# Optimization experiments

Measured on AMD Instinct MI355X. Metric: run time of the kernel, lower is better.

## Reference

```python
import jax, jax.numpy as jnp
import numpy as np

BN_EPS = 1e-5


def setup_inputs() -> dict:
    key = jax.random.key(0)
    ks = jax.random.split(key, 4)
    N, V, C = 64, 512, 512
    K, OUT = 2, 512
    x = jax.random.normal(ks[0], (N, V, C), dtype=jnp.float32)
    A = jax.random.uniform(ks[1], (N, K, V, V), dtype=jnp.float32) / V
    conv_w = jax.random.normal(ks[2], (2 * OUT, C), dtype=jnp.float32) / np.sqrt(C)
    conv_b = jax.random.normal(ks[3], (2 * OUT,), dtype=jnp.float32) * 0.01
    gamma = jnp.ones((2 * OUT,), dtype=jnp.float32)
    beta = jnp.zeros((2 * OUT,), dtype=jnp.float32)
    eps_p = jnp.zeros((1,), dtype=jnp.float32)
    return {"x": x, "A": A, "conv_w": conv_w, "conv_b": conv_b,
            "gamma": gamma, "beta": beta, "eps_p": eps_p}


def reference(x, A, conv_w, conv_b, gamma, beta, eps_p):
    # x: (N, V, C); A: (N, K, V, V)
    N, V, C = x.shape
    K = A.shape[1]
    # 1x1 Conv1d over nodes: (N, 2*out, V)
    h = jnp.einsum('nvc,oc->nov', x, conv_w) + conv_b[None, :, None]
    # BatchNorm1d, training-mode batch stats (biased variance, per channel)
    mean = jnp.mean(h, axis=(0, 2), keepdims=True)
    var = jnp.var(h, axis=(0, 2), keepdims=True)
    h = (h - mean) * jax.lax.rsqrt(var + BN_EPS) * gamma[None, :, None] + beta[None, :, None]
    c2 = h.shape[1]
    h = h.reshape(N, K, c2 // K, V)  # (N, K, out, V)
    # graph propagation: x A then (x A) A^T, contracted over node dims
    t = jnp.einsum('nkcm,nkme->nkce', h, A)
    At = jnp.transpose(A, (0, 1, 3, 2))
    y = jnp.einsum('nkce,nkem->ncm', t, At)  # (N, out, V)
    out = (1.0 + eps_p[0]) * x + jnp.transpose(y, (0, 2, 1))
    return out, At
```

## Files before the change

kernel.cpp:

```cpp
#include <hip/hip_runtime.h>
#include <stdint.h>

typedef __bf16 bf16x8 __attribute__((ext_vector_type(8)));
typedef float f32x4 __attribute__((ext_vector_type(4)));
typedef unsigned short us4_t __attribute__((ext_vector_type(4)));
typedef unsigned short us8_t __attribute__((ext_vector_type(8)));

__device__ __forceinline__ unsigned short f2bf(float f) {
  __bf16 b = (__bf16)f;
  return __builtin_bit_cast(unsigned short, b);
}
__device__ __forceinline__ float bf2f(unsigned short u) {
  union { uint32_t u; float f; } v; v.u = ((uint32_t)u) << 16;
  return v.f;
}

__device__ __forceinline__ void gload16(const void* g, void* l) {
  __builtin_amdgcn_global_load_lds(
      (const __attribute__((address_space(1))) void*)g,
      (__attribute__((address_space(3))) void*)l, 16, 0, 0);
}

__device__ __forceinline__ void stage_tile(const unsigned short* g, size_t ldg,
                                           unsigned short* lds, int wid, int lane) {
#pragma unroll
  for (int i = 0; i < 2; ++i) {
    int seg = wid * 2 + i;
    const unsigned short* gp = g + (size_t)(seg * 16 + (lane >> 2)) * ldg + (lane & 3) * 8;
    gload16(gp, lds + seg * 512);
  }
}

__device__ __forceinline__ void mfma_step(const unsigned short* As, const unsigned short* Bs,
                                          int ldb, f32x4 (*acc)[4],
                                          int wr, int wc, int lr, int lk) {
  bf16x8 a[4], b[4];
#pragma unroll
  for (int mi = 0; mi < 4; ++mi)
    a[mi] = *(const bf16x8*)(As + (wr + mi * 16 + lr) * 32 + lk * 8);
#pragma unroll
  for (int ni = 0; ni < 4; ++ni)
    b[ni] = *(const bf16x8*)(Bs + (wc + ni * 16 + lr) * ldb + lk * 8);
#pragma unroll
  for (int mi = 0; mi < 4; ++mi)
#pragma unroll
    for (int ni = 0; ni < 4; ++ni)
      acc[mi][ni] = __builtin_amdgcn_mfma_f32_16x16x32_bf16(a[mi], b[ni], acc[mi][ni], 0, 0, 0);
}

__device__ __forceinline__ void bn_block(
    const unsigned short* __restrict__ H, const float* __restrict__ gamma,
    const float* __restrict__ beta, float* __restrict__ sc_sh,
    int o, int tid, float* r1, float* r2) {
  const int g = tid >> 6, l = tid & 63;
  float s1 = 0.f, s2 = 0.f;
  for (int step = 0; step < 16; ++step) {
    int n = g + step * 4;
    const us8_t* row = (const us8_t*)(H + ((size_t)n * 1024 + o) * 512);
    us8_t v = row[l];
#pragma unroll
    for (int j = 0; j < 8; ++j) { float f = bf2f(v[j]); s1 += f; s2 += f * f; }
  }
  r1[tid] = s1; r2[tid] = s2;
  __syncthreads();
  for (int off = 128; off > 0; off >>= 1) {
    if (tid < off) { r1[tid] += r1[tid + off]; r2[tid] += r2[tid + off]; }
    __syncthreads();
  }
  if (tid == 0) {
    float mean = r1[0] * (1.0f / 32768.0f);
    float var = r2[0] * (1.0f / 32768.0f) - mean * mean;
    float s = gamma[o] * rsqrtf(var + 1e-5f);
    sc_sh[o] = s;
    sc_sh[1024 + o] = beta[o] - mean * s;
  }
}

__global__ __launch_bounds__(256) void k_convert(
    const float* __restrict__ X, const float* __restrict__ W,
    unsigned short* __restrict__ Xb, unsigned short* __restrict__ Wb) {
  const size_t idx = (size_t)blockIdx.x * 256 + threadIdx.x;
  const size_t stride = (size_t)gridDim.x * 256;
  for (size_t i = idx; i < (size_t)16777216 / 8; i += stride) {
    float4 f0 = ((const float4*)X)[2 * i], f1 = ((const float4*)X)[2 * i + 1];
    us8_t w = { f2bf(f0.x), f2bf(f0.y), f2bf(f0.z), f2bf(f0.w),
                f2bf(f1.x), f2bf(f1.y), f2bf(f1.z), f2bf(f1.w) };
    ((us8_t*)Xb)[i] = w;
  }
  for (size_t i = idx; i < (size_t)524288 / 8; i += stride) {
    float4 f0 = ((const float4*)W)[2 * i], f1 = ((const float4*)W)[2 * i + 1];
    us8_t w = { f2bf(f0.x), f2bf(f0.y), f2bf(f0.z), f2bf(f0.w),
                f2bf(f1.x), f2bf(f1.y), f2bf(f1.z), f2bf(f1.w) };
    ((us8_t*)Wb)[i] = w;
  }
}

__global__ __launch_bounds__(256) void k_gemm1(
    const unsigned short* __restrict__ Wb, const unsigned short* __restrict__ Xb,
    const float* __restrict__ convb, unsigned short* __restrict__ H) {
  __shared__ unsigned short As[4096];
  __shared__ unsigned short Bs[4096];
  const int tid = threadIdx.x;
  const int L = blockIdx.x;
  const int xcd = L & 7, slot = L >> 3;
  const int n = xcd * 8 + (slot >> 5);
  const int tile = slot & 31;
  const int tm = tile >> 2, tn = tile & 3;
  const unsigned short* gA = Wb + (size_t)tm * 128 * 512;
  const unsigned short* gB = Xb + ((size_t)n * 512 + tn * 128) * 512;
  const int lane = tid & 63, wid = tid >> 6;
  const int wr = (wid >> 1) * 64, wc = (wid & 1) * 64;
  const int lr = lane & 15, lk = lane >> 4;
  f32x4 acc[4][4] = {};
  for (int k0 = 0; k0 < 512; k0 += 32) {
    stage_tile(gA + k0, 512, As, wid, lane);
    stage_tile(gB + k0, 512, Bs, wid, lane);
    __syncthreads();
    mfma_step(As, Bs, 32, acc, wr, wc, lr, lk);
    __syncthreads();
  }
  unsigned short* Hn = H + (size_t)n * 1024 * 512;
#pragma unroll
  for (int mi = 0; mi < 4; ++mi)
#pragma unroll
    for (int i = 0; i < 4; ++i) {
      int o = tm * 128 + wr + mi * 16 + lk * 4 + i;
      float bias = convb[o];
#pragma unroll
      for (int ni = 0; ni < 4; ++ni) {
        int v = tn * 128 + wc + ni * 16 + lr;
        Hn[(size_t)o * 512 + v] = f2bf(acc[mi][ni][i] + bias);
      }
    }
}

__global__ __launch_bounds__(256) void k_bn_at_ab(
    const unsigned short* __restrict__ H, const float* __restrict__ gamma,
    const float* __restrict__ beta, float* __restrict__ sc_sh,
    const float* __restrict__ A, float* __restrict__ At,
    unsigned short* __restrict__ Ab) {
  const int tid = threadIdx.x;
  if (blockIdx.x < 1024) {
    __shared__ float r1[256], r2[256];
    bn_block(H, gamma, beta, sc_sh, blockIdx.x, tid, r1, r2);
  } else {
    __shared__ float tile[64][65];
    const int tIdx = blockIdx.x - 1024;
    const int nk = tIdx >> 6;
    const int e0 = (tIdx & 7) * 64, m0 = ((tIdx >> 3) & 7) * 64;
    const float* src = A + (size_t)nk * 262144;
    float* dst = At + (size_t)nk * 262144;
    unsigned short* ab = Ab + (size_t)nk * 262144;
#pragma unroll
    for (int j = 0; j < 4; ++j) {
      int ch = tid + j * 256;
      int r = ch >> 4, c4 = (ch & 15) * 4;
      float4 f = *(const float4*)(src + (size_t)(m0 + r) * 512 + e0 + c4);
      tile[r][c4] = f.x; tile[r][c4 + 1] = f.y; tile[r][c4 + 2] = f.z; tile[r][c4 + 3] = f.w;
      us4_t u = { f2bf(f.x), f2bf(f.y), f2bf(f.z), f2bf(f.w) };
      *(us4_t*)(ab + (size_t)(m0 + r) * 512 + e0 + c4) = u;
    }
    __syncthreads();
#pragma unroll
    for (int j = 0; j < 4; ++j) {
      int ch = tid + j * 256;
      int e = ch >> 4, m4 = (ch & 15) * 4;
      float4 g = { tile[m4][e], tile[m4 + 1][e], tile[m4 + 2][e], tile[m4 + 3][e] };
      *(float4*)(dst + (size_t)(e0 + e) * 512 + m0 + m4) = g;
    }
  }
}

__global__ __launch_bounds__(256) void k_bn_convA(
    const unsigned short* __restrict__ H, const float* __restrict__ gamma,
    const float* __restrict__ beta, float* __restrict__ sc_sh,
    const float* __restrict__ A, unsigned short* __restrict__ Ab) {
  const int tid = threadIdx.x;
  if (blockIdx.x < 1024) {
    __shared__ float r1[256], r2[256];
    bn_block(H, gamma, beta, sc_sh, blockIdx.x, tid, r1, r2);
  } else {
    const size_t idx = (size_t)(blockIdx.x - 1024) * 256 + tid;
    const size_t stride = (size_t)2048 * 256;
    for (size_t i = idx; i < (size_t)33554432 / 8; i += stride) {
      float4 f0 = ((const float4*)A)[2 * i], f1 = ((const float4*)A)[2 * i + 1];
      us8_t w = { f2bf(f0.x), f2bf(f0.y), f2bf(f0.z), f2bf(f0.w),
                  f2bf(f1.x), f2bf(f1.y), f2bf(f1.z), f2bf(f1.w) };
      ((us8_t*)Ab)[i] = w;
    }
  }
}

__global__ __launch_bounds__(256) void k_bn(
    const unsigned short* __restrict__ H, const float* __restrict__ gamma,
    const float* __restrict__ beta, float* __restrict__ sc_sh) {
  __shared__ float r1[256], r2[256];
  bn_block(H, gamma, beta, sc_sh, blockIdx.x, threadIdx.x, r1, r2);
}

__global__ __launch_bounds__(256) void k_convertA(
    const float* __restrict__ A, unsigned short* __restrict__ Ab) {
  const size_t idx = (size_t)blockIdx.x * 256 + threadIdx.x;
  const size_t stride = (size_t)gridDim.x * 256;
  for (size_t i = idx; i < (size_t)33554432 / 8; i += stride) {
    float4 f0 = ((const float4*)A)[2 * i], f1 = ((const float4*)A)[2 * i + 1];
    us8_t w = { f2bf(f0.x), f2bf(f0.y), f2bf(f0.z), f2bf(f0.w),
                f2bf(f1.x), f2bf(f1.y), f2bf(f1.z), f2bf(f1.w) };
    ((us8_t*)Ab)[i] = w;
  }
}

__global__ __launch_bounds__(256) void k_affine(
    unsigned short* __restrict__ H, const float* __restrict__ sc_sh) {
  const size_t idx = (size_t)blockIdx.x * 256 + threadIdx.x;
  const size_t stride = (size_t)gridDim.x * 256;
  const size_t total8 = (size_t)64 * 1024 * 512 / 8;
  for (size_t i = idx; i < total8; i += stride) {
    size_t base = i * 8;
    int o = (int)((base >> 9) & 1023);
    float sc = sc_sh[o], sh = sc_sh[1024 + o];
    us8_t v = ((const us8_t*)H)[i];
    us8_t w;
#pragma unroll
    for (int j = 0; j < 8; ++j) w[j] = f2bf(fmaf(bf2f(v[j]), sc, sh));
    ((us8_t*)H)[i] = w;
  }
}

__global__ __launch_bounds__(256) void k_aat(
    const unsigned short* __restrict__ Ab, unsigned short* __restrict__ B2) {
  __shared__ unsigned short As[4096];
  __shared__ unsigned short Bs[4096];
  const int tid = threadIdx.x;
  const int L = blockIdx.x;
  const int xcd = L & 7, slot = L >> 3;
  const int nk = xcd * 16 + (slot >> 4);
  const int tile = slot & 15;
  const int tm = tile >> 2, tn = tile & 3;
  const unsigned short* Ank = Ab + (size_t)nk * 262144;
  const unsigned short* gA = Ank + (size_t)tm * 128 * 512;
  const unsigned short* gB = Ank + (size_t)tn * 128 * 512;
  const int lane = tid & 63, wid = tid >> 6;
  const int wr = (wid >> 1) * 64, wc = (wid & 1) * 64;
  const int lr = lane & 15, lk = lane >> 4;
  f32x4 acc[4][4] = {};
  for (int k0 = 0; k0 < 512; k0 += 32) {
    stage_tile(gA + k0, 512, As, wid, lane);
    stage_tile(gB + k0, 512, Bs, wid, lane);
    __syncthreads();
    mfma_step(As, Bs, 32, acc, wr, wc, lr, lk);
    __syncthreads();
  }
  unsigned short* Bn = B2 + (size_t)nk * 262144;
#pragma unroll
  for (int mi = 0; mi < 4; ++mi)
#pragma unroll
    for (int i = 0; i < 4; ++i) {
      int m = tm * 128 + wr + mi * 16 + lk * 4 + i;
#pragma unroll
      for (int ni = 0; ni < 4; ++ni) {
        int mp = tn * 128 + wc + ni * 16 + lr;
        Bn[(size_t)m * 512 + mp] = f2bf(acc[mi][ni][i]);
      }
    }
}

__global__ __launch_bounds__(256) void k_aat_affine(
    const unsigned short* __restrict__ Ab, unsigned short* __restrict__ B2,
    unsigned short* __restrict__ H, const float* __restrict__ sc_sh) {
  const int tid = threadIdx.x;
  if (blockIdx.x >= 2048) {
    const size_t idx = (size_t)(blockIdx.x - 2048) * 256 + tid;
    const size_t stride = (size_t)2048 * 256;
    const size_t total8 = (size_t)64 * 1024 * 512 / 8;
    for (size_t i = idx; i < total8; i += stride) {
      size_t base = i * 8;
      int o = (int)((base >> 9) & 1023);
      float sc = sc_sh[o], sh = sc_sh[1024 + o];
      us8_t v = ((const us8_t*)H)[i];
      us8_t w;
#pragma unroll
      for (int j = 0; j < 8; ++j) w[j] = f2bf(fmaf(bf2f(v[j]), sc, sh));
      ((us8_t*)H)[i] = w;
    }
    return;
  }
  __shared__ unsigned short As[4096];
  __shared__ unsigned short Bs[4096];
  const int L = blockIdx.x;
  const int xcd = L & 7, slot = L >> 3;
  const int nk = xcd * 16 + (slot >> 4);
  const int tile = slot & 15;
  const int tm = tile >> 2, tn = tile & 3;
  const unsigned short* Ank = Ab + (size_t)nk * 262144;
  const unsigned short* gA = Ank + (size_t)tm * 128 * 512;
  const unsigned short* gB = Ank + (size_t)tn * 128 * 512;
  const int lane = tid & 63, wid = tid >> 6;
  const int wr = (wid >> 1) * 64, wc = (wid & 1) * 64;
  const int lr = lane & 15, lk = lane >> 4;
  f32x4 acc[4][4] = {};
  for (int k0 = 0; k0 < 512; k0 += 32) {
    stage_tile(gA + k0, 512, As, wid, lane);
    stage_tile(gB + k0, 512, Bs, wid, lane);
    __syncthreads();
    mfma_step(As, Bs, 32, acc, wr, wc, lr, lk);
    __syncthreads();
  }
  unsigned short* Bn = B2 + (size_t)nk * 262144;
#pragma unroll
  for (int mi = 0; mi < 4; ++mi)
#pragma unroll
    for (int i = 0; i < 4; ++i) {
      int m = tm * 128 + wr + mi * 16 + lk * 4 + i;
#pragma unroll
      for (int ni = 0; ni < 4; ++ni) {
        int mp = tn * 128 + wc + ni * 16 + lr;
        Bn[(size_t)m * 512 + mp] = f2bf(acc[mi][ni][i]);
      }
    }
}

__global__ __launch_bounds__(512) void k_gemm3(
    const unsigned short* __restrict__ B2, const unsigned short* __restrict__ H,
    const float* __restrict__ X, const float* __restrict__ epsp,
    float* __restrict__ out) {
  __shared__ unsigned short As[4096];
  __shared__ unsigned short Bs[4096];
  const int tid = threadIdx.x;
  const int L = blockIdx.x;
  const int xcd = L & 7, slot = L >> 3;
  const int n = xcd * 8 + (slot >> 4);
  const int tile = slot & 15;
  const int tm = tile >> 2, tn = tile & 3;
  const int lane = tid & 63, wid = tid >> 6;
  const int wr = (wid >> 2) * 64, wc = (wid & 3) * 32;
  const int lr = lane & 15, lk = lane >> 4;
  f32x4 acc[4][2] = {};
  for (int kk = 0; kk < 2; ++kk) {
    const unsigned short* gA = B2 + ((size_t)(n * 2 + kk) * 512 + tm * 128) * 512;
    const unsigned short* gB = H + ((size_t)n * 1024 + kk * 512 + tn * 128) * 512;
    for (int k0 = 0; k0 < 512; k0 += 32) {
      {
        int r = wid * 16 + (lane >> 2);
        int c = (lane & 3) * 8;
        gload16(gA + (size_t)r * 512 + k0 + c, As + wid * 512);
        gload16(gB + (size_t)r * 512 + k0 + c, Bs + wid * 512);
      }
      __syncthreads();
      bf16x8 a[4], b[2];
#pragma unroll
      for (int mi = 0; mi < 4; ++mi)
        a[mi] = *(const bf16x8*)(As + (wr + mi * 16 + lr) * 32 + lk * 8);
#pragma unroll
      for (int ni = 0; ni < 2; ++ni)
        b[ni] = *(const bf16x8*)(Bs + (wc + ni * 16 + lr) * 32 + lk * 8);
#pragma unroll
      for (int mi = 0; mi < 4; ++mi)
#pragma unroll
        for (int ni = 0; ni < 2; ++ni)
          acc[mi][ni] = __builtin_amdgcn_mfma_f32_16x16x32_bf16(a[mi], b[ni], acc[mi][ni], 0, 0, 0);
      __syncthreads();
    }
  }
  const float e1 = 1.0f + epsp[0];
#pragma unroll
  for (int mi = 0; mi < 4; ++mi)
#pragma unroll
    for (int i = 0; i < 4; ++i) {
      int v = tm * 128 + wr + mi * 16 + lk * 4 + i;
#pragma unroll
      for (int ni = 0; ni < 2; ++ni) {
        int c = tn * 128 + wc + ni * 16 + lr;
        size_t idx = ((size_t)n * 512 + v) * 512 + c;
        out[idx] = fmaf(e1, X[idx], acc[mi][ni][i]);
      }
    }
}

__global__ __launch_bounds__(256) void k_at(
    const float* __restrict__ A, float* __restrict__ At) {
  __shared__ float tile[64][65];
  const int nk = blockIdx.z;
  const int e0 = blockIdx.x * 64, m0 = blockIdx.y * 64;
  const float* src = A + (size_t)nk * 262144;
  float* dst = At + (size_t)nk * 262144;
  const int t = threadIdx.x;
#pragma unroll
  for (int j = 0; j < 4; ++j) {
    int ch = t + j * 256;
    int r = ch >> 4, c4 = (ch & 15) * 4;
    float4 f = *(const float4*)(src + (size_t)(m0 + r) * 512 + e0 + c4);
    tile[r][c4] = f.x; tile[r][c4 + 1] = f.y; tile[r][c4 + 2] = f.z; tile[r][c4 + 3] = f.w;
  }
  __syncthreads();
#pragma unroll
  for (int j = 0; j < 4; ++j) {
    int ch = t + j * 256;
    int e = ch >> 4, m4 = (ch & 15) * 4;
    float4 g = { tile[m4][e], tile[m4 + 1][e], tile[m4 + 2][e], tile[m4 + 3][e] };
    *(float4*)(dst + (size_t)(e0 + e) * 512 + m0 + m4) = g;
  }
}

extern "C" void kernel_launch(void* const* d_in, const int* in_sizes, int n_in,
                              void* d_out, int out_size, void* d_ws, size_t ws_size,
                              hipStream_t stream) {
  const float* x      = (const float*)d_in[0];
  const float* A      = (const float*)d_in[1];
  const float* conv_w = (const float*)d_in[2];
  const float* conv_b = (const float*)d_in[3];
  const float* gamma  = (const float*)d_in[4];
  const float* beta   = (const float*)d_in[5];
  const float* eps_p  = (const float*)d_in[6];

  float* out = (float*)d_out;
  float* At  = out + (size_t)16777216;

  unsigned short* Xb = (unsigned short*)out;
  unsigned short* Wb = Xb + (size_t)16777216;
  unsigned short* AbO = (unsigned short*)out;

  const size_t WS_BIG = (size_t)2 * 67108864 + 8192;
  if (ws_size >= WS_BIG) {
    unsigned short* H  = (unsigned short*)d_ws;
    unsigned short* B2 = H + (size_t)33554432;
    float* sc_sh = (float*)(B2 + (size_t)33554432);
    k_convert     <<<2048, 256, 0, stream>>>(x, conv_w, Xb, Wb);
    k_gemm1       <<<2048, 256, 0, stream>>>(Wb, Xb, conv_b, H);
    k_bn_at_ab    <<<9216, 256, 0, stream>>>(H, gamma, beta, sc_sh, A, At, AbO);
    k_aat_affine  <<<4096, 256, 0, stream>>>(AbO, B2, H, sc_sh);
    k_gemm3       <<<1024, 512, 0, stream>>>(B2, H, x, eps_p, out);
    return;
  }

  unsigned short* B2 = (unsigned short*)At;
  unsigned short* H  = (unsigned short*)(At + (size_t)16777216);
  float* wsf = (float*)d_ws;

  if (ws_size >= 8192) {
    float* sc_sh = wsf;
    k_convert     <<<2048, 256, 0, stream>>>(x, conv_w, Xb, Wb);
    k_gemm1       <<<2048, 256, 0, stream>>>(Wb, Xb, conv_b, H);
    k_bn_convA    <<<3072, 256, 0, stream>>>(H, gamma, beta, sc_sh, A, AbO);
    k_aat_affine  <<<4096, 256, 0, stream>>>(AbO, B2, H, sc_sh);
    k_gemm3       <<<1024, 512, 0, stream>>>(B2, H, x, eps_p, out);
  } else {
    float* sc_sh = out;
    k_convert     <<<2048, 256, 0, stream>>>(x, conv_w, Xb, Wb);
    k_gemm1       <<<2048, 256, 0, stream>>>(Wb, Xb, conv_b, H);
    k_bn          <<<1024, 256, 0, stream>>>(H, gamma, beta, sc_sh);
    k_affine      <<<2048, 256, 0, stream>>>(H, sc_sh);
    k_convertA    <<<2048, 256, 0, stream>>>(A, AbO);
    k_aat         <<<2048, 256, 0, stream>>>(AbO, B2);
    k_gemm3       <<<1024, 512, 0, stream>>>(B2, H, x, eps_p, out);
  }
  k_at<<<dim3(8, 8, 128), 256, 0, stream>>>(A, At);
}
```

Measured before the change: 280.6 us.

## Fuse A transpose/bf16 conversion into gemm1 launch when workspace allows

Adds a path for large workspaces where the A transpose and bf16 conversion blocks run in the same launch as the first GEMM, so this memory-bound work overlaps the compute-bound GEMM. BatchNorm statistics move to a separate k_bn kernel, and Ab goes into its own workspace region instead of aliasing the output buffer. The path only runs if the harness provides at least 3*64M bytes of workspace; otherwise the old path is used. Extra blocks may compete with the GEMM for bandwidth and CUs.

```diff
diff --git a/kernel.cpp b/kernel.cpp
--- a/kernel.cpp
+++ b/kernel.cpp
@@ -73,6 +73,33 @@
     float s = gamma[o] * rsqrtf(var + 1e-5f);
     sc_sh[o] = s;
     sc_sh[1024 + o] = beta[o] - mean * s;
+  }
+}
+
+__device__ __forceinline__ void at_ab_tile(
+    const float* __restrict__ A, float* __restrict__ At,
+    unsigned short* __restrict__ Ab, int tIdx, int tid, float (*tile)[65]) {
+  const int nk = tIdx >> 6;
+  const int e0 = (tIdx & 7) * 64, m0 = ((tIdx >> 3) & 7) * 64;
+  const float* src = A + (size_t)nk * 262144;
+  float* dst = At + (size_t)nk * 262144;
+  unsigned short* ab = Ab + (size_t)nk * 262144;
+#pragma unroll
+  for (int j = 0; j < 4; ++j) {
+    int ch = tid + j * 256;
+    int r = ch >> 4, c4 = (ch & 15) * 4;
+    float4 f = *(const float4*)(src + (size_t)(m0 + r) * 512 + e0 + c4);
+    tile[r][c4] = f.x; tile[r][c4 + 1] = f.y; tile[r][c4 + 2] = f.z; tile[r][c4 + 3] = f.w;
+    us4_t u = { f2bf(f.x), f2bf(f.y), f2bf(f.z), f2bf(f.w) };
+    *(us4_t*)(ab + (size_t)(m0 + r) * 512 + e0 + c4) = u;
+  }
+  __syncthreads();
+#pragma unroll
+  for (int j = 0; j < 4; ++j) {
+    int ch = tid + j * 256;
+    int e = ch >> 4, m4 = (ch & 15) * 4;
+    float4 g = { tile[m4][e], tile[m4 + 1][e], tile[m4 + 2][e], tile[m4 + 3][e] };
+    *(float4*)(dst + (size_t)(e0 + e) * 512 + m0 + m4) = g;
   }
 }
 
@@ -134,6 +161,52 @@
     }
 }
 
+__global__ __launch_bounds__(256) void k_gemm1_atab(
+    const unsigned short* __restrict__ Wb, const unsigned short* __restrict__ Xb,
+    const float* __restrict__ convb, unsigned short* __restrict__ H,
+    const float* __restrict__ A, float* __restrict__ At,
+    unsigned short* __restrict__ Ab) {
+  __shared__ __align__(16) char smem[64 * 65 * 4];
+  const int tid = threadIdx.x;
+  if (blockIdx.x >= 2048) {
+    at_ab_tile(A, At, Ab, blockIdx.x - 2048, tid, (float(*)[65])smem);
+    return;
+  }
+  unsigned short* As = (unsigned short*)smem;
+  unsigned short* Bs = As + 4096;
+  const int L = blockIdx.x;
+  const int xcd = L & 7, slot = L >> 3;
+  const int n = xcd * 8 + (slot >> 5);
+  const int tile = slot & 31;
+  const int tm = tile >> 2, tn = tile & 3;
+  const unsigned short* gA = Wb + (size_t)tm * 128 * 512;
+  const unsigned short* gB = Xb + ((size_t)n * 512 + tn * 128) * 512;
+  const int lane = tid & 63, wid = tid >> 6;
+  const int wr = (wid >> 1) * 64, wc = (wid & 1) * 64;
+  const int lr = lane & 15, lk = lane >> 4;
+  f32x4 acc[4][4] = {};
+  for (int k0 = 0; k0 < 512; k0 += 32) {
+    stage_tile(gA + k0, 512, As, wid, lane);
+    stage_tile(gB + k0, 512, Bs, wid, lane);
+    __syncthreads();
+    mfma_step(As, Bs, 32, acc, wr, wc, lr, lk);
+    __syncthreads();
+  }
+  unsigned short* Hn = H + (size_t)n * 1024 * 512;
+#pragma unroll
+  for (int mi = 0; mi < 4; ++mi)
+#pragma unroll
+    for (int i = 0; i < 4; ++i) {
+      int o = tm * 128 + wr + mi * 16 + lk * 4 + i;
+      float bias = convb[o];
+#pragma unroll
+      for (int ni = 0; ni < 4; ++ni) {
+        int v = tn * 128 + wc + ni * 16 + lr;
+        Hn[(size_t)o * 512 + v] = f2bf(acc[mi][ni][i] + bias);
+      }
+    }
+}
+
 __global__ __launch_bounds__(256) void k_bn_at_ab(
     const unsigned short* __restrict__ H, const float* __restrict__ gamma,
     const float* __restrict__ beta, float* __restrict__ sc_sh,
@@ -145,29 +218,7 @@
     bn_block(H, gamma, beta, sc_sh, blockIdx.x, tid, r1, r2);
   } else {
     __shared__ float tile[64][65];
-    const int tIdx = blockIdx.x - 1024;
-    const int nk = tIdx >> 6;
-    const int e0 = (tIdx & 7) * 64, m0 = ((tIdx >> 3) & 7) * 64;
-    const float* src = A + (size_t)nk * 262144;
-    float* dst = At + (size_t)nk * 262144;
-    unsigned short* ab = Ab + (size_t)nk * 262144;
-#pragma unroll
-    for (int j = 0; j < 4; ++j) {
-      int ch = tid + j * 256;
-      int r = ch >> 4, c4 = (ch & 15) * 4;
-      float4 f = *(const float4*)(src + (size_t)(m0 + r) * 512 + e0 + c4);
-      tile[r][c4] = f.x; tile[r][c4 + 1] = f.y; tile[r][c4 + 2] = f.z; tile[r][c4 + 3] = f.w;
-      us4_t u = { f2bf(f.x), f2bf(f.y), f2bf(f.z), f2bf(f.w) };
-      *(us4_t*)(ab + (size_t)(m0 + r) * 512 + e0 + c4) = u;
-    }
-    __syncthreads();
-#pragma unroll
-    for (int j = 0; j < 4; ++j) {
-      int ch = tid + j * 256;
-      int e = ch >> 4, m4 = (ch & 15) * 4;
-      float4 g = { tile[m4][e], tile[m4 + 1][e], tile[m4 + 2][e], tile[m4 + 3][e] };
-      *(float4*)(dst + (size_t)(e0 + e) * 512 + m0 + m4) = g;
-    }
+    at_ab_tile(A, At, Ab, blockIdx.x - 1024, tid, tile);
   }
 }
 
@@ -420,7 +471,21 @@
   unsigned short* Wb = Xb + (size_t)16777216;
   unsigned short* AbO = (unsigned short*)out;
 
+  const size_t WS_XL  = (size_t)3 * 67108864;
   const size_t WS_BIG = (size_t)2 * 67108864 + 8192;
+  if (ws_size >= WS_XL) {
+    unsigned short* H   = (unsigned short*)d_ws;
+    unsigned short* B2  = H + (size_t)33554432;
+    unsigned short* Abw = B2 + (size_t)33554432;
+    float* sc_sh = out;
+    k_convert     <<<2048,  256, 0, stream>>>(x, conv_w, Xb, Wb);
+    k_gemm1_atab  <<<10240, 256, 0, stream>>>(Wb, Xb, conv_b, H, A, At, Abw);
+    k_bn          <<<1024,  256, 0, stream>>>(H, gamma, beta, sc_sh);
+    k_aat_affine  <<<4096,  256, 0, stream>>>(Abw, B2, H, sc_sh);
+    k_gemm3       <<<1024,  512, 0, stream>>>(B2, H, x, eps_p, out);
+    return;
+  }
+
   if (ws_size >= WS_BIG) {
     unsigned short* H  = (unsigned short*)d_ws;
     unsigned short* B2 = H + (size_t)33554432;
```

Result: slower. 286.9 us (+2.2%).
